# Kernel tuning notes

Hardware: AMD Instinct MI355X
Metric: run time of the kernel (lower is better)

The kernel has to match this reference:

```python
import jax, jax.numpy as jnp
import numpy as np

N = 400000
H = 256          # hidden_dim
NUM_HEADS = 4
HEAD_DIM = H // NUM_HEADS
B = 1024         # number of graphs (segments)


def setup_inputs() -> dict:
    key = jax.random.key(0)
    ks = jax.random.split(key, 6)
    x = jax.random.normal(ks[0], (N, H), dtype=jnp.float32)
    batch = jnp.sort(jax.random.randint(ks[1], (N,), 0, B, dtype=jnp.int64))
    s = 1.0 / np.sqrt(H)
    W1 = jax.random.normal(ks[2], (H, H), dtype=jnp.float32) * s
    b1 = jnp.zeros((H,), dtype=jnp.float32)
    W2 = jax.random.normal(ks[3], (H, NUM_HEADS), dtype=jnp.float32) * s
    b2 = jnp.zeros((NUM_HEADS,), dtype=jnp.float32)
    Wt = jax.random.normal(ks[4], (H, H), dtype=jnp.float32) * s
    bt = jnp.zeros((H,), dtype=jnp.float32)
    return {"x": x, "batch": batch, "W1": W1, "b1": b1, "W2": W2, "b2": b2, "Wt": Wt, "bt": bt}


def reference(x, batch, W1, b1, W2, b2, Wt, bt):
    # attention MLP: Linear -> Tanh -> Linear  -> [N, num_heads]
    logits = jnp.tanh(x @ W1 + b1) @ W2 + b2
    # segment (per-graph) softmax over nodes, per head (PyG-style with 1e-16 eps)
    seg_max = jax.ops.segment_max(logits, batch, num_segments=B)        # [B, heads]
    e = jnp.exp(logits - seg_max[batch])                                # [N, heads]
    seg_sum = jax.ops.segment_sum(e, batch, num_segments=B)             # [B, heads]
    attn = e / (seg_sum[batch] + 1e-16)                                 # [N, heads]
    # transform + per-head weighting
    xt = (x @ Wt + bt).reshape(N, NUM_HEADS, HEAD_DIM)
    weighted = (attn[:, :, None] * xt).reshape(N, H)
    # global add pool over each graph
    graph_emb = jax.ops.segment_sum(weighted, batch, num_segments=B)    # [B, hidden]
    return graph_emb, attn
```

## Files before the change

kernel.cpp:

```cpp
#include <hip/hip_runtime.h>
#include <math.h>

#define HD    256
#define NHEAD 4
#define NSEG  1024
#define RPB   64
#define NRB64 6250

typedef short bf16x8 __attribute__((ext_vector_type(8)));
typedef float f32x16 __attribute__((ext_vector_type(16)));

__device__ __forceinline__ float tanh_fast(float v) {
    float e = __expf(2.0f * v);
    return 1.0f - 2.0f * __builtin_amdgcn_rcpf(e + 1.0f);
}

__device__ __forceinline__ void split2(float a, float b, unsigned &hi, unsigned &lo) {
    unsigned ba = __float_as_uint(a), bb = __float_as_uint(b);
    unsigned ha = ba & 0xFFFF0000u, hb = bb & 0xFFFF0000u;
    float la = a - __uint_as_float(ha);
    float lb = b - __uint_as_float(hb);
    hi = (ha >> 16) | hb;
    lo = (__float_as_uint(la) >> 16) | (__float_as_uint(lb) & 0xFFFF0000u);
}

__device__ __forceinline__ unsigned cvt_pk_bf16(float a, float b) {
    unsigned r;
    asm("v_cvt_pk_bf16_f32 %0, %1, %2" : "=v"(r) : "v"(a), "v"(b));
    return r;
}

__device__ __forceinline__ void gld16(const void* g, void* l) {
    __builtin_amdgcn_global_load_lds(
        (const __attribute__((address_space(1))) void*)g,
        (__attribute__((address_space(3))) void*)l, 16, 0, 0);
}

__global__ __launch_bounds__(256) void k0_prep(
    const float* __restrict__ W1, char* __restrict__ ws)
{
    int g = blockIdx.x * 256 + threadIdx.x;
    int c  = g & 127;
    int j  = (g >> 7) & 3;
    int o  = (g >> 9) & 1;
    int ch = (g >> 10) & 1;
    int t  = g >> 11;
    int k   = t*16 + o*8 + 2*j;
    int col = ch*128 + c;
    float a = W1[(size_t)k * HD + col];
    float b = W1[(size_t)(k + 1) * HD + col];
    unsigned hw, lw;
    split2(a, b, hw, lw);
    size_t off = (size_t)t*16384 + ch*8192 + o*2048 + c*16 + j*4;
    *(unsigned*)(ws + off)        = hw;
    *(unsigned*)(ws + off + 4096) = lw;
}

#define K1_THREADS 256
#define BUFB 12288
#define K1_LDS 32768

__global__ __launch_bounds__(K1_THREADS, 5) void k1_mfma(
    const float* __restrict__ x, const char* __restrict__ wsW,
    const float* __restrict__ b1, const float* __restrict__ W2,
    const float* __restrict__ b2, float* __restrict__ lgA,
    float* __restrict__ lgB, int N)
{
    extern __shared__ __align__(16) char smem[];

    const int raw = blockIdx.x;
    const int ch  = (raw >> 3) & 1;
    const int rb  = (raw >> 4) * 8 + (raw & 7);
    if (rb >= NRB64) return;

    const int tid  = threadIdx.x;
    const int lane = tid & 63;
    const int lo5  = lane & 31;
    const int hi   = lane >> 5;
    const int wid  = tid >> 6;
    const int rg   = wid >> 1;
    const int cg   = wid & 1;
    const int blkrow = rb * RPB;
    const int rl   = rg*32 + lo5;

    f32x16 acc[2];
    #pragma unroll
    for (int ct = 0; ct < 2; ++ct) {
        float b1v = b1[ch*128 + cg*64 + ct*32 + lo5];
        #pragma unroll
        for (int e = 0; e < 16; ++e) acc[ct][e] = b1v;
    }

    const char* gwbase = wsW + ch*8192 + tid*16;
    const char* gxbase;
    {
        int row  = tid >> 2;
        int slot = tid & 3;
        long grow = blkrow + row; if (grow > N-1) grow = N-1;
        gxbase = (const char*)x + grow*1024 + ((slot ^ (row & 3)) * 16);
    }

    auto STAGE = [&](int u) {
        const int db = (u & 1) * BUFB;
        const char* w = gwbase + (size_t)u*16384;
        #pragma unroll
        for (int i = 0; i < 2; ++i)
            gld16(w + i*4096, smem + db + i*4096 + tid*16);
        gld16(gxbase + (size_t)u*64, smem + db + 8192 + tid*16);
    };

    STAGE(0);
    __syncthreads();

    #pragma unroll
    for (int t = 0; t < 16; ++t) {
        if (t < 15) STAGE(t + 1);
        const int buf = (t & 1) * BUFB;
        {
            union { unsigned u[4]; bf16x8 v; } ah;
            {
                const int s0 = hi*2;
                const int xb = buf + 8192 + rl*64;
                float4 q0 = *(const float4*)(smem + xb + ((s0     ^ (rl & 3)) << 4));
                float4 q1 = *(const float4*)(smem + xb + (((s0+1) ^ (rl & 3)) << 4));
                ah.u[0] = cvt_pk_bf16(q0.x, q0.y);
                ah.u[1] = cvt_pk_bf16(q0.z, q0.w);
                ah.u[2] = cvt_pk_bf16(q1.x, q1.y);
                ah.u[3] = cvt_pk_bf16(q1.z, q1.w);
            }
            bf16x8 bh[2], bl[2];
            #pragma unroll
            for (int ct = 0; ct < 2; ++ct) {
                int off = buf + hi*2048 + (cg*64 + ct*32 + lo5)*16;
                bh[ct] = *(const bf16x8*)(smem + off);
                bl[ct] = *(const bf16x8*)(smem + off + 4096);
            }
            #pragma unroll
            for (int ct = 0; ct < 2; ++ct) {
                acc[ct] = __builtin_amdgcn_mfma_f32_32x32x16_bf16(ah.v, bh[ct], acc[ct], 0, 0, 0);
                acc[ct] = __builtin_amdgcn_mfma_f32_32x32x16_bf16(ah.v, bl[ct], acc[ct], 0, 0, 0);
            }
        }
        __syncthreads();
    }

    #pragma unroll
    for (int ct = 0; ct < 2; ++ct) {
        const int col = cg*64 + ct*32 + lo5;
        #pragma unroll
        for (int e = 0; e < 16; ++e) {
            float h = tanh_fast(acc[ct][e]);
            int row = rg*32 + (e & 3) + 8*(e >> 2) + 4*hi;
            unsigned hh = __float_as_uint(h) & 0xFFFF0000u;
            float hl = h - __uint_as_float(hh);
            int byte = row*256 + ((((col >> 3) ^ (row & 15))) << 4) + (col & 7)*2;
            *(unsigned short*)(smem + byte)         = (unsigned short)(hh >> 16);
            *(unsigned short*)(smem + 16384 + byte) = (unsigned short)(__float_as_uint(hl) >> 16);
        }
    }
    __syncthreads();

    f32x16 d;
    #pragma unroll
    for (int e = 0; e < 16; ++e) d[e] = 0.0f;
    const int rt_e  = wid;
    const int row_e = rt_e*32 + lo5;
    const int colh  = lo5 & 3;
    const bool act  = (wid < 2) && (lo5 < 4);
    if (wid < 2) {
        #pragma unroll
        for (int kk = 0; kk < 8; ++kk) {
            int sb = row_e*256 + (((kk*2 + hi) ^ (row_e & 15)) << 4);
            bf16x8 ahh = *(const bf16x8*)(smem + sb);
            bf16x8 alo = *(const bf16x8*)(smem + 16384 + sb);
            union { unsigned short s[8]; bf16x8 v; } wh, wl;
            #pragma unroll
            for (int j = 0; j < 8; ++j) {
                float w = W2[(size_t)(ch*128 + kk*16 + hi*8 + j)*NHEAD + colh];
                w = act ? w : 0.0f;
                unsigned hb = __float_as_uint(w) & 0xFFFF0000u;
                float wlf = w - __uint_as_float(hb);
                wh.s[j] = (unsigned short)(hb >> 16);
                wl.s[j] = (unsigned short)(__float_as_uint(wlf) >> 16);
            }
            d = __builtin_amdgcn_mfma_f32_32x32x16_bf16(ahh, wh.v, d, 0, 0, 0);
            d = __builtin_amdgcn_mfma_f32_32x32x16_bf16(ahh, wl.v, d, 0, 0, 0);
            d = __builtin_amdgcn_mfma_f32_32x32x16_bf16(alo, wh.v, d, 0, 0, 0);
        }
    }
    __syncthreads();

    float* p_lds = (float*)smem;
    if (act) {
        #pragma unroll
        for (int e = 0; e < 16; ++e) {
            int r = rt_e*32 + (e & 3) + 8*(e >> 2) + 4*hi;
            p_lds[r*4 + lo5] = d[e];
        }
    }
    __syncthreads();
    if (tid < RPB) {
        int grow = blkrow + tid;
        if (grow < N) {
            float4 o = *(float4*)(p_lds + tid*4);
            float* dst;
            if (ch == 0) {
                o.x += b2[0]; o.y += b2[1]; o.z += b2[2]; o.w += b2[3];
                dst = lgA;
            } else dst = lgB;
            *(float4*)(dst + (size_t)grow * NHEAD) = o;
        }
    }
}

__device__ __forceinline__ int lower_bound(const int* __restrict__ a, int n, int v) {
    int lo = 0, hi = n;
    while (lo < hi) { int m = (lo + hi) >> 1; if (a[m] < v) lo = m + 1; else hi = m; }
    return lo;
}

__global__ __launch_bounds__(256) void k2_seg(
    const int* __restrict__ batch, const float* __restrict__ lgA,
    const float* __restrict__ lgB, float* __restrict__ out, int N)
{
    const int b = blockIdx.x;
    const int tid = threadIdx.x;
    const int lane = tid & 63, wid = tid >> 6;
    const int start = lower_bound(batch, N, b);
    const int end   = lower_bound(batch, N, b + 1);
    const float4* la4 = (const float4*)lgA;
    const float4* lb4 = (const float4*)lgB;

    float4 mx = make_float4(-INFINITY, -INFINITY, -INFINITY, -INFINITY);
    for (int i = start + tid; i < end; i += 256) {
        float4 a = la4[i], bq = lb4[i];
        mx.x = fmaxf(mx.x, a.x + bq.x); mx.y = fmaxf(mx.y, a.y + bq.y);
        mx.z = fmaxf(mx.z, a.z + bq.z); mx.w = fmaxf(mx.w, a.w + bq.w);
    }
    #pragma unroll
    for (int ofs = 32; ofs >= 1; ofs >>= 1) {
        mx.x = fmaxf(mx.x, __shfl_xor(mx.x, ofs, 64));
        mx.y = fmaxf(mx.y, __shfl_xor(mx.y, ofs, 64));
        mx.z = fmaxf(mx.z, __shfl_xor(mx.z, ofs, 64));
        mx.w = fmaxf(mx.w, __shfl_xor(mx.w, ofs, 64));
    }
    __shared__ float4 red[4];
    if (lane == 0) red[wid] = mx;
    __syncthreads();
    float4 smax;
    smax.x = fmaxf(fmaxf(red[0].x, red[1].x), fmaxf(red[2].x, red[3].x));
    smax.y = fmaxf(fmaxf(red[0].y, red[1].y), fmaxf(red[2].y, red[3].y));
    smax.z = fmaxf(fmaxf(red[0].z, red[1].z), fmaxf(red[2].z, red[3].z));
    smax.w = fmaxf(fmaxf(red[0].w, red[1].w), fmaxf(red[2].w, red[3].w));
    __syncthreads();

    float4 sm = make_float4(0.f, 0.f, 0.f, 0.f);
    for (int i = start + tid; i < end; i += 256) {
        float4 a = la4[i], bq = lb4[i];
        sm.x += __expf(a.x + bq.x - smax.x); sm.y += __expf(a.y + bq.y - smax.y);
        sm.z += __expf(a.z + bq.z - smax.z); sm.w += __expf(a.w + bq.w - smax.w);
    }
    #pragma unroll
    for (int ofs = 32; ofs >= 1; ofs >>= 1) {
        sm.x += __shfl_xor(sm.x, ofs, 64);
        sm.y += __shfl_xor(sm.y, ofs, 64);
        sm.z += __shfl_xor(sm.z, ofs, 64);
        sm.w += __shfl_xor(sm.w, ofs, 64);
    }
    if (lane == 0) red[wid] = sm;
    __syncthreads();
    if (tid == 0) {
        float4 ssum;
        ssum.x = red[0].x + red[1].x + red[2].x + red[3].x;
        ssum.y = red[0].y + red[1].y + red[2].y + red[3].y;
        ssum.z = red[0].z + red[1].z + red[2].z + red[3].z;
        ssum.w = red[0].w + red[1].w + red[2].w + red[3].w;
        *(float4*)(out + (size_t)b * HD)     = smax;
        *(float4*)(out + (size_t)b * HD + 4) = ssum;
    }
}

__global__ __launch_bounds__(256) void k3_pool(
    const int* __restrict__ batch, const float* __restrict__ x,
    const float* __restrict__ Wt, const float* __restrict__ bt,
    const float* __restrict__ lgB, float* __restrict__ out, int N)
{
    const int b = blockIdx.x;
    const int tid = threadIdx.x;
    const int start = lower_bound(batch, N, b);
    const int end   = lower_bound(batch, N, b + 1);

    float4* at4 = (float4*)(out + (size_t)NSEG * HD);
    const float4* lb4 = (const float4*)lgB;

    const float4 smax = *(const float4*)(out + (size_t)b * HD);
    const float4 ssum = *(const float4*)(out + (size_t)b * HD + 4);
    float4 inv;
    inv.x = 1.0f / (ssum.x + 1e-16f); inv.y = 1.0f / (ssum.y + 1e-16f);
    inv.z = 1.0f / (ssum.z + 1e-16f); inv.w = 1.0f / (ssum.w + 1e-16f);

    float z0 = 0.f, z1 = 0.f, z2 = 0.f, z3 = 0.f;
    __shared__ float4 attn_s[256];

    for (int c0 = start; c0 < end; c0 += 256) {
        const int idx = c0 + tid;
        if (idx < end) {
            float4 l = at4[idx];
            float4 lb = lb4[idx];
            float4 a;
            a.x = __expf(l.x + lb.x - smax.x) * inv.x;
            a.y = __expf(l.y + lb.y - smax.y) * inv.y;
            a.z = __expf(l.z + lb.z - smax.z) * inv.z;
            a.w = __expf(l.w + lb.w - smax.w) * inv.w;
            at4[idx] = a;
            attn_s[tid] = a;
        }
        __syncthreads();
        const int cnt = min(256, end - c0);
        const float* xb = x + (size_t)c0 * HD + tid;
        #pragma unroll 4
        for (int i = 0; i < cnt; ++i) {
            float4 a = attn_s[i];
            float xv = xb[(size_t)i * HD];
            z0 = fmaf(a.x, xv, z0); z1 = fmaf(a.y, xv, z1);
            z2 = fmaf(a.z, xv, z2); z3 = fmaf(a.w, xv, z3);
        }
        __syncthreads();
    }

    __shared__ float zs[NHEAD][HD];
    zs[0][tid] = z0; zs[1][tid] = z1; zs[2][tid] = z2; zs[3][tid] = z3;
    __syncthreads();

    const int h = tid >> 6;
    float smh, invh;
    if      (h == 0) { smh = ssum.x; invh = inv.x; }
    else if (h == 1) { smh = ssum.y; invh = inv.y; }
    else if (h == 2) { smh = ssum.z; invh = inv.z; }
    else             { smh = ssum.w; invh = inv.w; }

    float acc = smh * invh * bt[tid];
    #pragma unroll 4
    for (int k = 0; k < HD; ++k)
        acc = fmaf(zs[h][k], Wt[(size_t)k * HD + tid], acc);

    out[(size_t)b * HD + tid] = acc;
}

extern "C" void kernel_launch(void* const* d_in, const int* in_sizes, int n_in,
                              void* d_out, int out_size, void* d_ws, size_t ws_size,
                              hipStream_t stream) {
    const float* x   = (const float*)d_in[0];
    const int*   bat = (const int*)  d_in[1];
    const float* W1  = (const float*)d_in[2];
    const float* b1  = (const float*)d_in[3];
    const float* W2  = (const float*)d_in[4];
    const float* b2  = (const float*)d_in[5];
    const float* Wt  = (const float*)d_in[6];
    const float* bt  = (const float*)d_in[7];
    float* out = (float*)d_out;
    const int N = in_sizes[0] / HD;

    float* lgA = out + (size_t)NSEG * HD;
    char*  wsW = (char*)d_ws;
    float* lgB = (float*)((char*)d_ws + 262144);

    hipLaunchKernelGGL(k0_prep, dim3(128), dim3(256), 0, stream, W1, wsW);
    hipLaunchKernelGGL(k1_mfma, dim3(((NRB64 + 7) / 8) * 16), dim3(K1_THREADS),
                       K1_LDS, stream, x, wsW, b1, W2, b2, lgA, lgB, N);
    hipLaunchKernelGGL(k2_seg, dim3(NSEG), dim3(256), 0, stream, bat, lgA, lgB, out, N);
    hipLaunchKernelGGL(k3_pool, dim3(NSEG), dim3(256), 0, stream, bat, x, Wt, bt, lgB, out, N);
}
```

Before: 334.7 us.

## Process second GEMM in two row passes with split-K across waves to cut LDS

The epilogue now stages the tanh output one 32-row group at a time instead of all 64 rows. This halves the LDS needed for the hidden staging buffer, which lets K1_LDS drop and launch bounds rise from 5 to 6 blocks per CU. The W2 projection is split across all four waves along K, with partial sums reduced through LDS, where before only two waves did the work. The cost is extra barriers and passes, a reduction step, and fewer threads writing outputs per pass.

```diff
diff --git a/kernel.cpp b/kernel.cpp
--- a/kernel.cpp
+++ b/kernel.cpp
@@ -58,9 +58,9 @@
 
 #define K1_THREADS 256
 #define BUFB 12288
-#define K1_LDS 32768
-
-__global__ __launch_bounds__(K1_THREADS, 5) void k1_mfma(
+#define K1_LDS 24576
+
+__global__ __launch_bounds__(K1_THREADS, 6) void k1_mfma(
     const float* __restrict__ x, const char* __restrict__ wsW,
     const float* __restrict__ b1, const float* __restrict__ W2,
     const float* __restrict__ b2, float* __restrict__ lgA,
@@ -144,71 +144,82 @@
         __syncthreads();
     }
 
-    #pragma unroll
-    for (int ct = 0; ct < 2; ++ct) {
-        const int col = cg*64 + ct*32 + lo5;
-        #pragma unroll
-        for (int e = 0; e < 16; ++e) {
-            float h = tanh_fast(acc[ct][e]);
-            int row = rg*32 + (e & 3) + 8*(e >> 2) + 4*hi;
-            unsigned hh = __float_as_uint(h) & 0xFFFF0000u;
-            float hl = h - __uint_as_float(hh);
-            int byte = row*256 + ((((col >> 3) ^ (row & 15))) << 4) + (col & 7)*2;
-            *(unsigned short*)(smem + byte)         = (unsigned short)(hh >> 16);
-            *(unsigned short*)(smem + 16384 + byte) = (unsigned short)(__float_as_uint(hl) >> 16);
-        }
-    }
-    __syncthreads();
-
-    f32x16 d;
-    #pragma unroll
-    for (int e = 0; e < 16; ++e) d[e] = 0.0f;
-    const int rt_e  = wid;
-    const int row_e = rt_e*32 + lo5;
-    const int colh  = lo5 & 3;
-    const bool act  = (wid < 2) && (lo5 < 4);
-    if (wid < 2) {
-        #pragma unroll
-        for (int kk = 0; kk < 8; ++kk) {
-            int sb = row_e*256 + (((kk*2 + hi) ^ (row_e & 15)) << 4);
-            bf16x8 ahh = *(const bf16x8*)(smem + sb);
-            bf16x8 alo = *(const bf16x8*)(smem + 16384 + sb);
-            union { unsigned short s[8]; bf16x8 v; } wh, wl;
-            #pragma unroll
-            for (int j = 0; j < 8; ++j) {
-                float w = W2[(size_t)(ch*128 + kk*16 + hi*8 + j)*NHEAD + colh];
-                w = act ? w : 0.0f;
-                unsigned hb = __float_as_uint(w) & 0xFFFF0000u;
-                float wlf = w - __uint_as_float(hb);
-                wh.s[j] = (unsigned short)(hb >> 16);
-                wl.s[j] = (unsigned short)(__float_as_uint(wlf) >> 16);
-            }
-            d = __builtin_amdgcn_mfma_f32_32x32x16_bf16(ahh, wh.v, d, 0, 0, 0);
-            d = __builtin_amdgcn_mfma_f32_32x32x16_bf16(ahh, wl.v, d, 0, 0, 0);
-            d = __builtin_amdgcn_mfma_f32_32x32x16_bf16(alo, wh.v, d, 0, 0, 0);
-        }
-    }
-    __syncthreads();
-
-    float* p_lds = (float*)smem;
-    if (act) {
-        #pragma unroll
-        for (int e = 0; e < 16; ++e) {
-            int r = rt_e*32 + (e & 3) + 8*(e >> 2) + 4*hi;
-            p_lds[r*4 + lo5] = d[e];
-        }
-    }
-    __syncthreads();
-    if (tid < RPB) {
-        int grow = blkrow + tid;
-        if (grow < N) {
-            float4 o = *(float4*)(p_lds + tid*4);
-            float* dst;
-            if (ch == 0) {
-                o.x += b2[0]; o.y += b2[1]; o.z += b2[2]; o.w += b2[3];
-                dst = lgA;
-            } else dst = lgB;
-            *(float4*)(dst + (size_t)grow * NHEAD) = o;
+    float* p_par = (float*)(smem + 16384);
+    #pragma unroll
+    for (int p = 0; p < 2; ++p) {
+        __syncthreads();
+        if (rg == p) {
+            #pragma unroll
+            for (int ct = 0; ct < 2; ++ct) {
+                const int col = cg*64 + ct*32 + lo5;
+                #pragma unroll
+                for (int e = 0; e < 16; ++e) {
+                    float h = tanh_fast(acc[ct][e]);
+                    int row = (e & 3) + 8*(e >> 2) + 4*hi;
+                    unsigned hh = __float_as_uint(h) & 0xFFFF0000u;
+                    float hl = h - __uint_as_float(hh);
+                    int byte = row*256 + ((((col >> 3) ^ (row & 15))) << 4) + (col & 7)*2;
+                    *(unsigned short*)(smem + byte)        = (unsigned short)(hh >> 16);
+                    *(unsigned short*)(smem + 8192 + byte) = (unsigned short)(__float_as_uint(hl) >> 16);
+                }
+            }
+        }
+        __syncthreads();
+        {
+            const int row  = lo5;
+            const int colh = lo5 & 3;
+            const bool act = lo5 < 4;
+            f32x16 d;
+            #pragma unroll
+            for (int e = 0; e < 16; ++e) d[e] = 0.0f;
+            #pragma unroll
+            for (int kq = 0; kq < 2; ++kq) {
+                const int kk = wid*2 + kq;
+                int sb = row*256 + (((kk*2 + hi) ^ (row & 15)) << 4);
+                bf16x8 ahh = *(const bf16x8*)(smem + sb);
+                bf16x8 alo = *(const bf16x8*)(smem + 8192 + sb);
+                union { unsigned short s[8]; bf16x8 v; } wh, wl;
+                #pragma unroll
+                for (int j = 0; j < 8; ++j) {
+                    float w = W2[(size_t)(ch*128 + kk*16 + hi*8 + j)*NHEAD + colh];
+                    w = act ? w : 0.0f;
+                    unsigned hb = __float_as_uint(w) & 0xFFFF0000u;
+                    float wlf = w - __uint_as_float(hb);
+                    wh.s[j] = (unsigned short)(hb >> 16);
+                    wl.s[j] = (unsigned short)(__float_as_uint(wlf) >> 16);
+                }
+                d = __builtin_amdgcn_mfma_f32_32x32x16_bf16(ahh, wh.v, d, 0, 0, 0);
+                d = __builtin_amdgcn_mfma_f32_32x32x16_bf16(ahh, wl.v, d, 0, 0, 0);
+                d = __builtin_amdgcn_mfma_f32_32x32x16_bf16(alo, wh.v, d, 0, 0, 0);
+            }
+            if (act) {
+                #pragma unroll
+                for (int e = 0; e < 16; ++e) {
+                    int r = (e & 3) + 8*(e >> 2) + 4*hi;
+                    p_par[(wid*32 + r)*4 + lo5] = d[e];
+                }
+            }
+        }
+        __syncthreads();
+        if (tid < 32) {
+            int grow = blkrow + p*32 + tid;
+            if (grow < N) {
+                float4 o0 = *(float4*)(p_par + (0*32 + tid)*4);
+                float4 o1 = *(float4*)(p_par + (1*32 + tid)*4);
+                float4 o2 = *(float4*)(p_par + (2*32 + tid)*4);
+                float4 o3 = *(float4*)(p_par + (3*32 + tid)*4);
+                float4 o;
+                o.x = o0.x + o1.x + o2.x + o3.x;
+                o.y = o0.y + o1.y + o2.y + o3.y;
+                o.z = o0.z + o1.z + o2.z + o3.z;
+                o.w = o0.w + o1.w + o2.w + o3.w;
+                float* dst;
+                if (ch == 0) {
+                    o.x += b2[0]; o.y += b2[1]; o.z += b2[2]; o.w += b2[3];
+                    dst = lgA;
+                } else dst = lgB;
+                *(float4*)(dst + (size_t)grow * NHEAD) = o;
+            }
         }
     }
 }
```

Measured after the change: 431.6 us. 1.29x slower.
